# Kernel optimization log

Hardware: AMD Instinct MI355X
Metric: run time of the kernel (lower is better)

The kernel has to match this reference:

```python
import jax, jax.numpy as jnp
import numpy as np

BN_EPS = 1e-5


def sparse_conv(feats, pin, pout, W, n_out):
    # gather-GEMM-scatter: feats [N_in, C], pin/pout [K, P], W [K, C, D]
    contrib = jnp.einsum('kpc,kcd->kpd', feats[pin], W)  # [K, P, D]
    D = W.shape[-1]
    out = jnp.zeros((n_out, D), feats.dtype)
    return out.at[pout.reshape(-1)].add(contrib.reshape(-1, D))


def bn_relu(x, g, b):
    # BatchNorm1d in training mode over the point dim (biased variance)
    m = x.mean(axis=0)
    v = jnp.var(x, axis=0)
    return jax.nn.relu((x - m) * jax.lax.rsqrt(v + BN_EPS) * g + b)


def setup_inputs() -> dict:
    key = jax.random.key(0)
    ks = jax.random.split(key, 12)
    N_in, N_out, K = 200000, 50000, 27
    P1, P2 = 100000, 30000
    Cin, Cout = 32, 64
    inp = {
        'feats': jax.random.normal(ks[0], (N_in, Cin), jnp.float32),
        'W_down': jax.random.normal(ks[1], (K, Cin, Cout), jnp.float32) * 0.05,
        'g0': jnp.ones((Cout,), jnp.float32),
        'b0': jnp.zeros((Cout,), jnp.float32),
        'W1': jax.random.normal(ks[2], (K, Cout, Cout), jnp.float32) * 0.05,
        'g1': jnp.ones((Cout,), jnp.float32),
        'b1': jnp.zeros((Cout,), jnp.float32),
        'W2': jax.random.normal(ks[3], (K, Cout, Cout), jnp.float32) * 0.05,
        'g2': jnp.ones((Cout,), jnp.float32),
        'b2': jnp.zeros((Cout,), jnp.float32),
        'pairs_down_in': jax.random.randint(ks[4], (K, P1), 0, N_in, jnp.int32),
        'pairs_down_out': jax.random.randint(ks[5], (K, P1), 0, N_out, jnp.int32),
        'pairs_subm_in': jax.random.randint(ks[6], (K, P2), 0, N_out, jnp.int32),
        'pairs_subm_out': jax.random.randint(ks[7], (K, P2), 0, N_out, jnp.int32),
        'n_out': N_out,
    }
    return inp


def reference(feats, W_down, g0, b0, W1, g1, b1, W2, g2, b2,
              pairs_down_in, pairs_down_out, pairs_subm_in, pairs_subm_out, n_out):
    # DownBlock: strided sparse conv + BN + ReLU
    x = bn_relu(sparse_conv(feats, pairs_down_in, pairs_down_out, W_down, n_out), g0, b0)
    # ResBlock: two submanifold convs sharing one pair map (same indice_key)
    x_net = bn_relu(sparse_conv(x, pairs_subm_in, pairs_subm_out, W1, n_out), g1, b1)
    res = bn_relu(sparse_conv(x_net, pairs_subm_in, pairs_subm_out, W2, n_out), g2, b2)
    return x_net + res
```

## Files before the change

kernel.cpp:

```cpp
#include <hip/hip_runtime.h>
#include <hip/hip_bf16.h>

#define K_TAPS 27
#define DCH 64
#define BN_EPS 1e-5f
#define SCAN_CHUNK 4096

typedef float f32x4 __attribute__((ext_vector_type(4)));
typedef short bf16x8 __attribute__((ext_vector_type(8)));
typedef unsigned int uint;

#define CVTPK(dst, lo, hi) \
    asm("v_cvt_pk_bf16_f32 %0, %1, %2" : "=v"(dst) : "v"(lo), "v"(hi))

__global__ __launch_bounds__(256)
void rank_kernel(const int* __restrict__ pout, int P,
                 int* __restrict__ counts, uint* __restrict__ packed)
{
    const int k = blockIdx.y;
    const int p = blockIdx.x * 256 + threadIdx.x;
    if (p < P) {
        const size_t i = (size_t)k * P + p;
        const int b = pout[i] * K_TAPS + k;
        const int r = atomicAdd(&counts[b], 1);
        packed[i] = ((uint)b << 11) | (uint)(r & 2047);
    }
}

__global__ __launch_bounds__(256)
void scan_sum_kernel(const int* __restrict__ counts, int n, int* __restrict__ partials)
{
    __shared__ int sm[256];
    const int base = blockIdx.x * SCAN_CHUNK;
    int s = 0;
#pragma unroll
    for (int j = 0; j < 16; ++j) {
        const int i = base + j * 256 + threadIdx.x;
        if (i < n) s += counts[i];
    }
    sm[threadIdx.x] = s;
    __syncthreads();
    for (int off = 128; off > 0; off >>= 1) {
        if (threadIdx.x < off) sm[threadIdx.x] += sm[threadIdx.x + off];
        __syncthreads();
    }
    if (threadIdx.x == 0) partials[blockIdx.x] = sm[0];
}

__global__ __launch_bounds__(512)
void scan_partials_kernel(int* __restrict__ partials, int n)
{
    __shared__ int sm[512];
    const int t = threadIdx.x;
    const int v = (t < n) ? partials[t] : 0;
    sm[t] = v;
    __syncthreads();
    for (int off = 1; off < 512; off <<= 1) {
        int tv = 0;
        if (t >= off) tv = sm[t - off];
        __syncthreads();
        if (t >= off) sm[t] += tv;
        __syncthreads();
    }
    if (t < n) partials[t] = sm[t] - v;
}

__global__ __launch_bounds__(256)
void scan_write_kernel(const int* __restrict__ counts, int n,
                       const int* __restrict__ chunkoff, int* __restrict__ S)
{
    __shared__ int sm[256];
    const int base = blockIdx.x * SCAN_CHUNK + threadIdx.x * 16;
    int v[16];
    int s = 0;
#pragma unroll
    for (int j = 0; j < 16; ++j) {
        const int i = base + j;
        v[j] = (i < n) ? counts[i] : 0;
        s += v[j];
    }
    sm[threadIdx.x] = s;
    __syncthreads();
    for (int off = 1; off < 256; off <<= 1) {
        int tv = 0;
        if (threadIdx.x >= off) tv = sm[threadIdx.x - off];
        __syncthreads();
        if (threadIdx.x >= off) sm[threadIdx.x] += tv;
        __syncthreads();
    }
    int run = chunkoff[blockIdx.x] + sm[threadIdx.x] - s;
#pragma unroll
    for (int j = 0; j < 16; ++j) {
        const int i = base + j;
        if (i < n) {
            S[i] = run;
            run += v[j];
            if (i == n - 1) S[n] = run;
        }
    }
}

__global__ __launch_bounds__(256)
void scatter_kernel(const int* __restrict__ pin, const uint* __restrict__ packed,
                    int P, const int* __restrict__ S, int* __restrict__ E)
{
    const int k = blockIdx.y;
    const int p = blockIdx.x * 256 + threadIdx.x;
    if (p < P) {
        const size_t i = (size_t)k * P + p;
        const uint u = packed[i];
        E[S[u >> 11] + (int)(u & 2047u)] = pin[i];
    }
}

__global__ __launch_bounds__(256)
void pack_w_kernel(const float* __restrict__ Wd,
                   const float* __restrict__ W1,
                   const float* __restrict__ W2,
                   uint* __restrict__ Pd, uint* __restrict__ P1, uint* __restrict__ P2)
{
    int b = blockIdx.x;
    const float* W; uint* P; int C, k;
    if (b < 27)      { W = Wd; P = Pd; C = 32; k = b; }
    else if (b < 54) { W = W1; P = P1; C = 64; k = b - 27; }
    else             { W = W2; P = P2; C = 64; k = b - 54; }
    const int KC = C / 32;
    for (int t = threadIdx.x; t < KC * 4 * 64; t += 256) {
        const int l  = t & 63;
        const int nt = (t >> 6) & 3;
        const int kc = t >> 8;
        const int c0  = kc * 32 + ((l >> 4) << 3);
        const int col = nt * 16 + (l & 15);
        float f[8];
#pragma unroll
        for (int j = 0; j < 8; ++j)
            f[j] = W[((size_t)k * C + c0 + j) * DCH + col];
        uint4 u;
        CVTPK(u.x, f[0], f[1]);
        CVTPK(u.y, f[2], f[3]);
        CVTPK(u.z, f[4], f[5]);
        CVTPK(u.w, f[6], f[7]);
        *reinterpret_cast<uint4*>(P + ((size_t)((k * KC + kc) * 4 + nt) * 64 + l) * 4) = u;
    }
}

template <int C>
__global__ __launch_bounds__(256, 4)
void mfma_conv_kernel(const float* __restrict__ x,
                      const uint* __restrict__ Wp,
                      const int* __restrict__ S,
                      const int* __restrict__ E,
                      float* __restrict__ y,
                      float* __restrict__ stats,
                      int n_out)
{
    constexpr int KC = C / 32;
    constexpr int SN = 16 * K_TAPS + 1;
    const int lane = threadIdx.x & 63;
    const int wave = threadIdx.x >> 6;
    const int r0 = blockIdx.x * 64 + wave * 16;
    if (r0 >= n_out) return;

    __shared__ int sS[4][SN];
    {
        const int base = r0 * K_TAPS;
        for (int i = lane; i < SN; i += 64) sS[wave][i] = S[base + i];
    }

    const int l15  = lane & 15;
    const int kgrp = lane >> 4;
    const int koff = kgrp * 8;

    f32x4 acc[4];
#pragma unroll
    for (int nt = 0; nt < 4; ++nt) acc[nt] = (f32x4)0.f;

    for (int k = 0; k < K_TAPS; ++k) {
        bf16x8 B[KC][4];
#pragma unroll
        for (int kc = 0; kc < KC; ++kc)
#pragma unroll
            for (int nt = 0; nt < 4; ++nt)
                B[kc][nt] = *reinterpret_cast<const bf16x8*>(
                    Wp + ((size_t)((k * KC + kc) * 4 + nt) * 64 + lane) * 4);

        const int e0 = sS[wave][l15 * K_TAPS + k];
        const int e1 = sS[wave][l15 * K_TAPS + k + 1];
        int s = 0;
        while (__any(e0 + s < e1)) {
            const bool alive = (e0 + s < e1);
            const int irow = alive ? E[e0 + s] : 0;
            bf16x8 a[KC];
#pragma unroll
            for (int kc = 0; kc < KC; ++kc) {
                float4 f0 = {0.f, 0.f, 0.f, 0.f}, f1 = {0.f, 0.f, 0.f, 0.f};
                if (alive) {
                    const float4* fp = reinterpret_cast<const float4*>(
                        x + (size_t)irow * C + kc * 32 + koff);
                    f0 = fp[0];
                    f1 = fp[1];
                }
                uint4 u;
                CVTPK(u.x, f0.x, f0.y);
                CVTPK(u.y, f0.z, f0.w);
                CVTPK(u.z, f1.x, f1.y);
                CVTPK(u.w, f1.z, f1.w);
                a[kc] = *reinterpret_cast<bf16x8*>(&u);
            }
#pragma unroll
            for (int kc = 0; kc < KC; ++kc)
#pragma unroll
                for (int nt = 0; nt < 4; ++nt)
                    acc[nt] = __builtin_amdgcn_mfma_f32_16x16x32_bf16(
                        a[kc], B[kc][nt], acc[nt], 0, 0, 0);
            ++s;
        }
    }

#pragma unroll
    for (int nt = 0; nt < 4; ++nt) {
        const int col = nt * 16 + l15;
        float sum = 0.f, ssum = 0.f;
#pragma unroll
        for (int j = 0; j < 4; ++j) {
            const float v = acc[nt][j];
            y[(size_t)(r0 + kgrp * 4 + j) * DCH + col] = v;
            sum += v;
            ssum += v * v;
        }
        sum  += __shfl_xor(sum, 16);  sum  += __shfl_xor(sum, 32);
        ssum += __shfl_xor(ssum, 16); ssum += __shfl_xor(ssum, 32);
        if (kgrp == 0) {
            unsafeAtomicAdd(&stats[col], sum);
            unsafeAtomicAdd(&stats[64 + col], ssum);
        }
    }
}

__global__ __launch_bounds__(256)
void bn_apply_kernel(float* __restrict__ x, int n_elem,
                     const float* __restrict__ stats,
                     const float* __restrict__ g,
                     const float* __restrict__ b,
                     float inv_n)
{
    const int d = threadIdx.x & 63;
    const float m   = stats[d] * inv_n;
    const float var = stats[64 + d] * inv_n - m * m;
    const float sc  = g[d] * rsqrtf(var + BN_EPS);
    const float sh  = b[d] - m * sc;
    for (int i = blockIdx.x * 256 + threadIdx.x; i < n_elem; i += gridDim.x * 256) {
        float v = x[i];
        x[i] = fmaxf(__builtin_fmaf(v, sc, sh), 0.f);
    }
}

__global__ __launch_bounds__(256)
void bn_final_kernel(float* __restrict__ y2, const float* __restrict__ xnet,
                     int n_elem,
                     const float* __restrict__ stats,
                     const float* __restrict__ g,
                     const float* __restrict__ b,
                     float inv_n)
{
    const int d = threadIdx.x & 63;
    const float m   = stats[d] * inv_n;
    const float var = stats[64 + d] * inv_n - m * m;
    const float sc  = g[d] * rsqrtf(var + BN_EPS);
    const float sh  = b[d] - m * sc;
    for (int i = blockIdx.x * 256 + threadIdx.x; i < n_elem; i += gridDim.x * 256) {
        float v = y2[i];
        y2[i] = xnet[i] + fmaxf(__builtin_fmaf(v, sc, sh), 0.f);
    }
}

extern "C" void kernel_launch(void* const* d_in, const int* in_sizes, int n_in,
                              void* d_out, int out_size, void* d_ws, size_t ws_size,
                              hipStream_t stream)
{
    const float* feats  = (const float*)d_in[0];
    const float* W_down = (const float*)d_in[1];
    const float* g0     = (const float*)d_in[2];
    const float* b0     = (const float*)d_in[3];
    const float* W1     = (const float*)d_in[4];
    const float* g1     = (const float*)d_in[5];
    const float* b1     = (const float*)d_in[6];
    const float* W2     = (const float*)d_in[7];
    const float* g2     = (const float*)d_in[8];
    const float* b2     = (const float*)d_in[9];
    const int* pdi      = (const int*)d_in[10];
    const int* pdo      = (const int*)d_in[11];
    const int* psi      = (const int*)d_in[12];
    const int* pso      = (const int*)d_in[13];

    const int P1     = in_sizes[10] / K_TAPS;
    const int P2     = in_sizes[12] / K_TAPS;
    const int M1     = in_sizes[10];
    const int n_out  = out_size / DCH;
    const int n_elem = n_out * DCH;
    const int NB     = n_out * K_TAPS;
    const float inv_n = 1.0f / (float)n_out;

    float* out = (float*)d_out;

    float* xnet  = (float*)d_ws;
    int*   counts = (int*)d_ws;
    uint*  rank_sm = (uint*)d_ws + NB;
    float* stats = xnet + (size_t)n_elem;
    int* S = (int*)(stats + 384);
    int* E = S + (NB + 1);
    int* partials = E + M1;
    uint* Wp_dn = (uint*)(partials + 1024);
    uint* Wp_s1 = Wp_dn + 27 * 1 * 4 * 64 * 4;
    uint* Wp_s2 = Wp_s1 + 27 * 2 * 4 * 64 * 4;
    uint* rank_dn = (uint*)d_out;

    float* st0 = stats;
    float* st1 = stats + 128;
    float* st2 = stats + 256;

    const dim3 blk(256);
    const dim3 gridH1((P1 + 255) / 256, K_TAPS);
    const dim3 gridH2((P2 + 255) / 256, K_TAPS);
    const int nchunks = (NB + SCAN_CHUNK - 1) / SCAN_CHUNK;
    const int ewBlocks = 2048;
    const int convBlocks = (n_out + 63) / 64;

    hipMemsetAsync(stats, 0, sizeof(float) * 384, stream);

    pack_w_kernel<<<81, blk, 0, stream>>>(W_down, W1, W2, Wp_dn, Wp_s1, Wp_s2);

    hipMemsetAsync(counts, 0, sizeof(int) * (size_t)NB, stream);
    rank_kernel<<<gridH1, blk, 0, stream>>>(pdo, P1, counts, rank_dn);
    scan_sum_kernel<<<nchunks, blk, 0, stream>>>(counts, NB, partials);
    scan_partials_kernel<<<1, 512, 0, stream>>>(partials, nchunks);
    scan_write_kernel<<<nchunks, blk, 0, stream>>>(counts, NB, partials, S);
    scatter_kernel<<<gridH1, blk, 0, stream>>>(pdi, rank_dn, P1, S, E);

    mfma_conv_kernel<32><<<convBlocks, blk, 0, stream>>>(feats, Wp_dn, S, E, out, st0, n_out);
    bn_apply_kernel<<<ewBlocks, blk, 0, stream>>>(out, n_elem, st0, g0, b0, inv_n);

    hipMemsetAsync(counts, 0, sizeof(int) * (size_t)NB, stream);
    rank_kernel<<<gridH2, blk, 0, stream>>>(pso, P2, counts, rank_sm);
    scan_sum_kernel<<<nchunks, blk, 0, stream>>>(counts, NB, partials);
    scan_partials_kernel<<<1, 512, 0, stream>>>(partials, nchunks);
    scan_write_kernel<<<nchunks, blk, 0, stream>>>(counts, NB, partials, S);
    scatter_kernel<<<gridH2, blk, 0, stream>>>(psi, rank_sm, P2, S, E);

    mfma_conv_kernel<64><<<convBlocks, blk, 0, stream>>>(out, Wp_s1, S, E, xnet, st1, n_out);
    bn_apply_kernel<<<ewBlocks, blk, 0, stream>>>(xnet, n_elem, st1, g1, b1, inv_n);

    mfma_conv_kernel<64><<<convBlocks, blk, 0, stream>>>(xnet, Wp_s2, S, E, out, st2, n_out);

    bn_final_kernel<<<ewBlocks, blk, 0, stream>>>(out, xnet, n_elem, st2, g2, b2, inv_n);
}
```

Measured before the change: 786.7 us.

## Gather bf16 activations in sparse conv and split taps across two waves

Adds a pre-conversion of the input features to bf16, and BN kernels now also write a bf16 copy of their output. The conv gathers then read half the bytes per row and skip in-loop conversion. The conv kernel is restructured to 128-thread blocks of 16 output rows, with the two waves splitting the 27 taps and reducing accumulators through shared memory. This shortens each wave's dependent gather loop and raises block count. The costs are an extra conversion pass over the input features, extra bf16 writes in BN, an LDS reduction, and a fallback that depends on workspace size.

```diff
diff --git a/kernel.cpp b/kernel.cpp
--- a/kernel.cpp
+++ b/kernel.cpp
@@ -9,6 +9,7 @@
 typedef float f32x4 __attribute__((ext_vector_type(4)));
 typedef short bf16x8 __attribute__((ext_vector_type(8)));
 typedef unsigned int uint;
+typedef unsigned short ushort;
 
 #define CVTPK(dst, lo, hi) \
     asm("v_cvt_pk_bf16_f32 %0, %1, %2" : "=v"(dst) : "v"(lo), "v"(hi))
@@ -144,9 +145,20 @@
     }
 }
 
-template <int C>
-__global__ __launch_bounds__(256, 4)
-void mfma_conv_kernel(const float* __restrict__ x,
+__global__ __launch_bounds__(256)
+void f2bf_kernel(const float* __restrict__ in, uint* __restrict__ out, int n_half)
+{
+    for (int i = blockIdx.x * 256 + threadIdx.x; i < n_half; i += gridDim.x * 256) {
+        const float2 v = reinterpret_cast<const float2*>(in)[i];
+        uint u;
+        CVTPK(u, v.x, v.y);
+        out[i] = u;
+    }
+}
+
+template <int C, typename T>
+__global__ __launch_bounds__(128, 5)
+void mfma_conv_kernel(const T* __restrict__ x,
                       const uint* __restrict__ Wp,
                       const int* __restrict__ S,
                       const int* __restrict__ E,
@@ -156,16 +168,17 @@
 {
     constexpr int KC = C / 32;
     constexpr int SN = 16 * K_TAPS + 1;
-    const int lane = threadIdx.x & 63;
-    const int wave = threadIdx.x >> 6;
-    const int r0 = blockIdx.x * 64 + wave * 16;
+    const int tid  = threadIdx.x;
+    const int lane = tid & 63;
+    const int wave = tid >> 6;
+    const int r0 = blockIdx.x * 16;
     if (r0 >= n_out) return;
 
-    __shared__ int sS[4][SN];
-    {
-        const int base = r0 * K_TAPS;
-        for (int i = lane; i < SN; i += 64) sS[wave][i] = S[base + i];
-    }
+    __shared__ int sS[SN];
+    __shared__ f32x4 red[2][4][64];
+
+    for (int i = tid; i < SN; i += 128) sS[i] = S[r0 * K_TAPS + i];
+    __syncthreads();
 
     const int l15  = lane & 15;
     const int kgrp = lane >> 4;
@@ -175,7 +188,7 @@
 #pragma unroll
     for (int nt = 0; nt < 4; ++nt) acc[nt] = (f32x4)0.f;
 
-    for (int k = 0; k < K_TAPS; ++k) {
+    for (int k = wave; k < K_TAPS; k += 2) {
         bf16x8 B[KC][4];
 #pragma unroll
         for (int kc = 0; kc < KC; ++kc)
@@ -184,8 +197,8 @@
                 B[kc][nt] = *reinterpret_cast<const bf16x8*>(
                     Wp + ((size_t)((k * KC + kc) * 4 + nt) * 64 + lane) * 4);
 
-        const int e0 = sS[wave][l15 * K_TAPS + k];
-        const int e1 = sS[wave][l15 * K_TAPS + k + 1];
+        const int e0 = sS[l15 * K_TAPS + k];
+        const int e1 = sS[l15 * K_TAPS + k + 1];
         int s = 0;
         while (__any(e0 + s < e1)) {
             const bool alive = (e0 + s < e1);
@@ -193,19 +206,27 @@
             bf16x8 a[KC];
 #pragma unroll
             for (int kc = 0; kc < KC; ++kc) {
-                float4 f0 = {0.f, 0.f, 0.f, 0.f}, f1 = {0.f, 0.f, 0.f, 0.f};
-                if (alive) {
-                    const float4* fp = reinterpret_cast<const float4*>(
-                        x + (size_t)irow * C + kc * 32 + koff);
-                    f0 = fp[0];
-                    f1 = fp[1];
+                if constexpr (sizeof(T) == 2) {
+                    bf16x8 av = (bf16x8)0;
+                    if (alive)
+                        av = *reinterpret_cast<const bf16x8*>(
+                            (const ushort*)x + (size_t)irow * C + kc * 32 + koff);
+                    a[kc] = av;
+                } else {
+                    float4 f0 = {0.f, 0.f, 0.f, 0.f}, f1 = {0.f, 0.f, 0.f, 0.f};
+                    if (alive) {
+                        const float4* fp = reinterpret_cast<const float4*>(
+                            (const float*)x + (size_t)irow * C + kc * 32 + koff);
+                        f0 = fp[0];
+                        f1 = fp[1];
+                    }
+                    uint4 u;
+                    CVTPK(u.x, f0.x, f0.y);
+                    CVTPK(u.y, f0.z, f0.w);
+                    CVTPK(u.z, f1.x, f1.y);
+                    CVTPK(u.w, f1.z, f1.w);
+                    a[kc] = *reinterpret_cast<bf16x8*>(&u);
                 }
-                uint4 u;
-                CVTPK(u.x, f0.x, f0.y);
-                CVTPK(u.y, f0.z, f0.w);
-                CVTPK(u.z, f1.x, f1.y);
-                CVTPK(u.w, f1.z, f1.w);
-                a[kc] = *reinterpret_cast<bf16x8*>(&u);
             }
 #pragma unroll
             for (int kc = 0; kc < KC; ++kc)
@@ -218,12 +239,18 @@
     }
 
 #pragma unroll
-    for (int nt = 0; nt < 4; ++nt) {
+    for (int nt = 0; nt < 4; ++nt) red[wave][nt][lane] = acc[nt];
+    __syncthreads();
+
+#pragma unroll
+    for (int t = 0; t < 2; ++t) {
+        const int nt = wave * 2 + t;
+        const f32x4 v4 = red[0][nt][lane] + red[1][nt][lane];
         const int col = nt * 16 + l15;
         float sum = 0.f, ssum = 0.f;
 #pragma unroll
         for (int j = 0; j < 4; ++j) {
-            const float v = acc[nt][j];
+            const float v = v4[j];
             y[(size_t)(r0 + kgrp * 4 + j) * DCH + col] = v;
             sum += v;
             ssum += v * v;
@@ -237,21 +264,30 @@
     }
 }
 
-__global__ __launch_bounds__(256)
-void bn_apply_kernel(float* __restrict__ x, int n_elem,
+template <bool WB>
+__global__ __launch_bounds__(256)
+void bn_apply_kernel(float* __restrict__ x, uint* __restrict__ xb, int n_half,
                      const float* __restrict__ stats,
                      const float* __restrict__ g,
                      const float* __restrict__ b,
                      float inv_n)
 {
-    const int d = threadIdx.x & 63;
-    const float m   = stats[d] * inv_n;
-    const float var = stats[64 + d] * inv_n - m * m;
-    const float sc  = g[d] * rsqrtf(var + BN_EPS);
-    const float sh  = b[d] - m * sc;
-    for (int i = blockIdx.x * 256 + threadIdx.x; i < n_elem; i += gridDim.x * 256) {
-        float v = x[i];
-        x[i] = fmaxf(__builtin_fmaf(v, sc, sh), 0.f);
+    const int d0 = (threadIdx.x * 2) & 63;
+    const float m0 = stats[d0] * inv_n,     m1 = stats[d0 + 1] * inv_n;
+    const float v0 = stats[64 + d0] * inv_n - m0 * m0;
+    const float v1 = stats[64 + d0 + 1] * inv_n - m1 * m1;
+    const float sc0 = g[d0] * rsqrtf(v0 + BN_EPS), sc1 = g[d0 + 1] * rsqrtf(v1 + BN_EPS);
+    const float sh0 = b[d0] - m0 * sc0,            sh1 = b[d0 + 1] - m1 * sc1;
+    for (int i = blockIdx.x * 256 + threadIdx.x; i < n_half; i += gridDim.x * 256) {
+        float2 v = reinterpret_cast<float2*>(x)[i];
+        const float r0 = fmaxf(__builtin_fmaf(v.x, sc0, sh0), 0.f);
+        const float r1 = fmaxf(__builtin_fmaf(v.y, sc1, sh1), 0.f);
+        reinterpret_cast<float2*>(x)[i] = make_float2(r0, r1);
+        if (WB) {
+            uint u;
+            CVTPK(u, r0, r1);
+            xb[i] = u;
+        }
     }
 }
 
@@ -296,6 +332,7 @@
     const int P1     = in_sizes[10] / K_TAPS;
     const int P2     = in_sizes[12] / K_TAPS;
     const int M1     = in_sizes[10];
+    const int Nin    = in_sizes[0] / 32;
     const int n_out  = out_size / DCH;
     const int n_elem = n_out * DCH;
     const int NB     = n_out * K_TAPS;
@@ -315,20 +352,31 @@
     uint* Wp_s2 = Wp_s1 + 27 * 2 * 4 * 64 * 4;
     uint* rank_dn = (uint*)d_out;
 
+    uintptr_t pa = (uintptr_t)(Wp_s2 + 27 * 2 * 4 * 64 * 4);
+    pa = (pa + 15) & ~(uintptr_t)15;
+    uint* featsb = (uint*)pa;
+    uint* x0b    = featsb + (size_t)Nin * 16;
+    uint* xnetb  = x0b + (size_t)n_elem / 2;
+    const size_t needed = (size_t)((char*)(xnetb + n_elem / 2) - (char*)d_ws);
+    const bool bf16path = ws_size >= needed;
+
     float* st0 = stats;
     float* st1 = stats + 128;
     float* st2 = stats + 256;
 
     const dim3 blk(256);
+    const dim3 cblk(128);
     const dim3 gridH1((P1 + 255) / 256, K_TAPS);
     const dim3 gridH2((P2 + 255) / 256, K_TAPS);
     const int nchunks = (NB + SCAN_CHUNK - 1) / SCAN_CHUNK;
     const int ewBlocks = 2048;
-    const int convBlocks = (n_out + 63) / 64;
+    const int convBlocks = (n_out + 15) / 16;
 
     hipMemsetAsync(stats, 0, sizeof(float) * 384, stream);
 
     pack_w_kernel<<<81, blk, 0, stream>>>(W_down, W1, W2, Wp_dn, Wp_s1, Wp_s2);
+    if (bf16path)
+        f2bf_kernel<<<ewBlocks, blk, 0, stream>>>(feats, featsb, Nin * 16);
 
     hipMemsetAsync(counts, 0, sizeof(int) * (size_t)NB, stream);
     rank_kernel<<<gridH1, blk, 0, stream>>>(pdo, P1, counts, rank_dn);
@@ -337,8 +385,16 @@
     scan_write_kernel<<<nchunks, blk, 0, stream>>>(counts, NB, partials, S);
     scatter_kernel<<<gridH1, blk, 0, stream>>>(pdi, rank_dn, P1, S, E);
 
-    mfma_conv_kernel<32><<<convBlocks, blk, 0, stream>>>(feats, Wp_dn, S, E, out, st0, n_out);
-    bn_apply_kernel<<<ewBlocks, blk, 0, stream>>>(out, n_elem, st0, g0, b0, inv_n);
+    if (bf16path)
+        mfma_conv_kernel<32, ushort><<<convBlocks, cblk, 0, stream>>>(
+            (const ushort*)featsb, Wp_dn, S, E, out, st0, n_out);
+    else
+        mfma_conv_kernel<32, float><<<convBlocks, cblk, 0, stream>>>(
+            feats, Wp_dn, S, E, out, st0, n_out);
+    if (bf16path)
+        bn_apply_kernel<true><<<ewBlocks, blk, 0, stream>>>(out, x0b, n_elem / 2, st0, g0, b0, inv_n);
+    else
+        bn_apply_kernel<false><<<ewBlocks, blk, 0, stream>>>(out, nullptr, n_elem / 2, st0, g0, b0, inv_n);
 
     hipMemsetAsync(counts, 0, sizeof(int) * (size_t)NB, stream);
     rank_kernel<<<gridH2, blk, 0, stream>>>(pso, P2, counts, rank_sm);
@@ -347,10 +403,23 @@
     scan_write_kernel<<<nchunks, blk, 0, stream>>>(counts, NB, partials, S);
     scatter_kernel<<<gridH2, blk, 0, stream>>>(psi, rank_sm, P2, S, E);
 
-    mfma_conv_kernel<64><<<convBlocks, blk, 0, stream>>>(out, Wp_s1, S, E, xnet, st1, n_out);
-    bn_apply_kernel<<<ewBlocks, blk, 0, stream>>>(xnet, n_elem, st1, g1, b1, inv_n);
-
-    mfma_conv_kernel<64><<<convBlocks, blk, 0, stream>>>(xnet, Wp_s2, S, E, out, st2, n_out);
+    if (bf16path)
+        mfma_conv_kernel<64, ushort><<<convBlocks, cblk, 0, stream>>>(
+            (const ushort*)x0b, Wp_s1, S, E, xnet, st1, n_out);
+    else
+        mfma_conv_kernel<64, float><<<convBlocks, cblk, 0, stream>>>(
+            out, Wp_s1, S, E, xnet, st1, n_out);
+    if (bf16path)
+        bn_apply_kernel<true><<<ewBlocks, blk, 0, stream>>>(xnet, xnetb, n_elem / 2, st1, g1, b1, inv_n);
+    else
+        bn_apply_kernel<false><<<ewBlocks, blk, 0, stream>>>(xnet, nullptr, n_elem / 2, st1, g1, b1, inv_n);
+
+    if (bf16path)
+        mfma_conv_kernel<64, ushort><<<convBlocks, cblk, 0, stream>>>(
+            (const ushort*)xnetb, Wp_s2, S, E, out, st2, n_out);
+    else
+        mfma_conv_kernel<64, float><<<convBlocks, cblk, 0, stream>>>(
+            xnet, Wp_s2, S, E, out, st2, n_out);
 
     bn_final_kernel<<<ewBlocks, blk, 0, stream>>>(out, xnet, n_elem, st2, g2, b2, inv_n);
 }
```

Measured after the change: 687.8 us. 12.6% less time.
